# Optimization experiments

Hardware: AMD Instinct MI355X
Metric: run time of the kernel (lower is better)

Reference implementation:

```python
import jax, jax.numpy as jnp
import numpy as np

N_HEAD, D_MODEL, D_K, D_V = 16, 1024, 64, 64
B, L = 8, 1024
NEG = -1000000000.0
EPS = 1e-6


def setup_inputs() -> dict:
    key = jax.random.key(0)
    ks = jax.random.split(key, 8)
    s = 0.02
    return {
        "q": jax.random.normal(ks[0], (B, L, D_MODEL), jnp.float32),
        "k": jax.random.normal(ks[1], (B, L, D_MODEL), jnp.float32),
        "v": jax.random.normal(ks[2], (B, L, D_MODEL), jnp.float32),
        "mask": jnp.ones((B, L, L), jnp.int32),
        "w_q": jax.random.normal(ks[3], (D_MODEL, N_HEAD * D_K), jnp.float32) * s,
        "w_k": jax.random.normal(ks[4], (D_MODEL, N_HEAD * D_K), jnp.float32) * s,
        "w_v": jax.random.normal(ks[5], (D_MODEL, N_HEAD * D_V), jnp.float32) * s,
        "w_o": jax.random.normal(ks[6], (N_HEAD * D_V, D_MODEL), jnp.float32) * s,
        "gamma": jnp.ones((D_MODEL,), jnp.float32),
        "beta": jnp.zeros((D_MODEL,), jnp.float32),
    }


def reference(q, k, v, mask, w_q, w_k, w_v, w_o, gamma, beta):
    residual = q
    scale = D_K ** 0.5
    # project and split heads: [B, H, L, d]
    qh = (q @ w_q).reshape(B, L, N_HEAD, D_K).transpose(0, 2, 1, 3)
    kh = (k @ w_k).reshape(B, L, N_HEAD, D_K).transpose(0, 2, 1, 3)
    vh = (v @ w_v).reshape(B, L, N_HEAD, D_V).transpose(0, 2, 1, 3)
    scores = jnp.einsum('bhqd,bhkd->bhqk', qh / scale, kh)
    scores = jnp.where(mask[:, None, :, :] == 0, NEG, scores)
    attn = jax.nn.softmax(scores, axis=-1)  # dropout = identity (eval)
    ctx = jnp.einsum('bhqk,bhkd->bhqd', attn, vh)
    ctx = ctx.transpose(0, 2, 1, 3).reshape(B, L, N_HEAD * D_V)
    out = ctx @ w_o + residual
    mu = jnp.mean(out, axis=-1, keepdims=True)
    var = jnp.var(out, axis=-1, keepdims=True)
    out = (out - mu) / jnp.sqrt(var + EPS) * gamma + beta
    return out, attn
```

## Files before the change

### kernel.cpp

```cpp
#include <hip/hip_runtime.h>

typedef __bf16 bf16_t;
typedef __bf16 bf16x8 __attribute__((ext_vector_type(8)));
typedef float f32x4 __attribute__((ext_vector_type(4)));

#define MFMA16(a, b, c) __builtin_amdgcn_mfma_f32_16x16x32_bf16((a), (b), (c), 0, 0, 0)

__device__ __forceinline__ bf16_t f2b(float f) { return (bf16_t)f; }

__global__ __launch_bounds__(256) void prep_kernel(
    const float* __restrict__ w0, const float* __restrict__ w1,
    const float* __restrict__ w2, const float* __restrict__ w3,
    bf16_t* __restrict__ WT)
{
    int z = blockIdx.z;
    const float* W = (z == 0) ? w0 : (z == 1) ? w1 : (z == 2) ? w2 : w3;
    bf16_t* dst = WT + ((size_t)z << 20);
    __shared__ float lds[64 * 65];
    int n0 = blockIdx.x * 64, c0 = blockIdx.y * 64;
    int t = threadIdx.x;
    int rl = t >> 2, q4 = t & 3;
    const float* src = W + (size_t)(c0 + rl) * 1024 + n0 + q4 * 16;
    float4 a0 = *(const float4*)(src);
    float4 a1 = *(const float4*)(src + 4);
    float4 a2 = *(const float4*)(src + 8);
    float4 a3 = *(const float4*)(src + 12);
    float* lr = lds + rl * 65 + q4 * 16;
    lr[0] = a0.x; lr[1] = a0.y; lr[2] = a0.z; lr[3] = a0.w;
    lr[4] = a1.x; lr[5] = a1.y; lr[6] = a1.z; lr[7] = a1.w;
    lr[8] = a2.x; lr[9] = a2.y; lr[10] = a2.z; lr[11] = a2.w;
    lr[12] = a3.x; lr[13] = a3.y; lr[14] = a3.z; lr[15] = a3.w;
    __syncthreads();
    bf16x8 o0, o1;
#pragma unroll
    for (int j = 0; j < 8; ++j) o0[j] = f2b(lds[(q4 * 16 + j) * 65 + rl]);
#pragma unroll
    for (int j = 0; j < 8; ++j) o1[j] = f2b(lds[(q4 * 16 + 8 + j) * 65 + rl]);
    bf16_t* dp = dst + (size_t)(n0 + rl) * 1024 + c0 + q4 * 16;
    *(bf16x8*)(dp) = o0;
    *(bf16x8*)(dp + 8) = o1;
}

__global__ __launch_bounds__(256) void gemm_kernel(
    const float* __restrict__ Aq, const float* __restrict__ Ak,
    const float* __restrict__ Av, const bf16_t* __restrict__ Actx,
    const bf16_t* __restrict__ WT,
    bf16_t* __restrict__ oq, bf16_t* __restrict__ ok, bf16_t* __restrict__ ovT,
    float* __restrict__ otmp, int mode_base)
{
    int mode = mode_base + blockIdx.z;
    const float* Af = (mode == 0) ? Aq : (mode == 1) ? Ak : Av;
    const bf16_t* Wp = WT + ((size_t)mode << 20);
    __shared__ __align__(16) unsigned char sm[16384];
    int m0 = blockIdx.y * 128, n0 = blockIdx.x * 128;
    int t = threadIdx.x;
    int srow = t >> 1, shalf = t & 1;
    int wv = t >> 6, lane = t & 63, lrow = lane & 15, g = lane >> 4;
    int wm = (wv >> 1) * 64, wn = (wv & 1) * 64;
    f32x4 acc[4][4] = {};
    for (int kt = 0; kt < 32; ++kt) {
        int k0 = kt * 32;
        __syncthreads();
        {
            unsigned sab = srow * 64;
            int ch0 = (shalf * 2) ^ (srow & 3), ch1 = (shalf * 2 + 1) ^ (srow & 3);
            if (mode < 3) {
                const float* s = Af + (size_t)(m0 + srow) * 1024 + k0 + shalf * 16;
                float4 f0 = *(const float4*)(s);
                float4 f1 = *(const float4*)(s + 4);
                float4 f2 = *(const float4*)(s + 8);
                float4 f3 = *(const float4*)(s + 12);
                bf16x8 p0 = {f2b(f0.x), f2b(f0.y), f2b(f0.z), f2b(f0.w),
                             f2b(f1.x), f2b(f1.y), f2b(f1.z), f2b(f1.w)};
                bf16x8 p1 = {f2b(f2.x), f2b(f2.y), f2b(f2.z), f2b(f2.w),
                             f2b(f3.x), f2b(f3.y), f2b(f3.z), f2b(f3.w)};
                *(bf16x8*)(sm + sab + ch0 * 16) = p0;
                *(bf16x8*)(sm + sab + ch1 * 16) = p1;
            } else {
                const bf16_t* s = Actx + (size_t)(m0 + srow) * 1024 + k0 + shalf * 16;
                *(bf16x8*)(sm + sab + ch0 * 16) = *(const bf16x8*)(s);
                *(bf16x8*)(sm + sab + ch1 * 16) = *(const bf16x8*)(s + 8);
            }
            const bf16_t* sb = Wp + (size_t)(n0 + srow) * 1024 + k0 + shalf * 16;
            *(bf16x8*)(sm + 8192 + sab + ch0 * 16) = *(const bf16x8*)(sb);
            *(bf16x8*)(sm + 8192 + sab + ch1 * 16) = *(const bf16x8*)(sb + 8);
        }
        __syncthreads();
        bf16x8 av[4], bv[4];
#pragma unroll
        for (int i = 0; i < 4; ++i) {
            int ra = wm + i * 16 + lrow;
            av[i] = *(const bf16x8*)(sm + ra * 64 + ((g ^ (ra & 3)) * 16));
            int rb = wn + i * 16 + lrow;
            bv[i] = *(const bf16x8*)(sm + 8192 + rb * 64 + ((g ^ (rb & 3)) * 16));
        }
#pragma unroll
        for (int i = 0; i < 4; ++i)
#pragma unroll
            for (int j = 0; j < 4; ++j)
                acc[i][j] = MFMA16(av[i], bv[j], acc[i][j]);
    }
#pragma unroll
    for (int i = 0; i < 4; ++i)
#pragma unroll
        for (int j = 0; j < 4; ++j)
#pragma unroll
            for (int r = 0; r < 4; ++r) {
                int m = m0 + wm + i * 16 + 4 * g + r;
                int n = n0 + wn + j * 16 + lrow;
                float vv = acc[i][j][r];
                if (mode == 3) {
                    otmp[(size_t)m * 1024 + n] = vv;
                } else {
                    int b = m >> 10, l = m & 1023, h = n >> 6, d = n & 63;
                    int bh = (b << 4) | h;
                    if (mode == 0)
                        oq[((size_t)bh * 1024 + l) * 64 + d] = f2b(vv);
                    else if (mode == 1)
                        ok[((size_t)bh * 1024 + l) * 64 + d] = f2b(vv);
                    else
                        ovT[(size_t)bh * 65536 + (size_t)(l >> 5) * 2048 + d * 32 + (l & 31)] = f2b(vv);
                }
            }
}

__global__ __launch_bounds__(512) void attn_kernel(
    const bf16_t* __restrict__ wq, const bf16_t* __restrict__ wk,
    const bf16_t* __restrict__ wvT, const int* __restrict__ mask,
    float* __restrict__ attn, bf16_t* __restrict__ ctxo)
{
    __shared__ __align__(16) unsigned char sm[139264];
    int qt = blockIdx.x, bh = blockIdx.y;
    int b = bh >> 4, h = bh & 15;
    int t = threadIdx.x, wv = t >> 6, lane = t & 63, lrow = lane & 15, g = lane >> 4;
    const bf16_t* Kb = wk + (size_t)bh * 65536;
#pragma unroll
    for (int it = 0; it < 16; ++it) {
        int cid = it * 512 + t;
        int krow = cid >> 3, ch = cid & 7;
        *(bf16x8*)(sm + krow * 128 + ((ch ^ (krow & 7)) * 16)) =
            *(const bf16x8*)(Kb + krow * 64 + ch * 8);
    }
    __syncthreads();
    int q0 = qt * 128 + wv * 16;
    const bf16_t* Qb = wq + ((size_t)bh * 1024 + q0 + lrow) * 64;
    bf16x8 aq0 = *(const bf16x8*)(Qb + 8 * g);
    bf16x8 aq1 = *(const bf16x8*)(Qb + 32 + 8 * g);
    const int* mrow = mask + ((size_t)b * 1024 + q0) * 1024;
    f32x4 zf = {0.f, 0.f, 0.f, 0.f};
    float denom[4] = {0.f, 0.f, 0.f, 0.f};
    for (int kt = 0; kt < 64; ++kt) {
        int kc = kt * 16 + lrow;
        unsigned kb = kc * 128;
        bf16x8 bk0 = *(const bf16x8*)(sm + kb + ((g ^ (kc & 7)) * 16));
        bf16x8 bk1 = *(const bf16x8*)(sm + kb + (((4 + g) ^ (kc & 7)) * 16));
        f32x4 s = MFMA16(aq0, bk0, zf);
        s = MFMA16(aq1, bk1, s);
#pragma unroll
        for (int r = 0; r < 4; ++r) {
            float e = mrow[(size_t)(4 * g + r) * 1024 + kc] ? __expf(0.125f * s[r]) : 0.f;
            denom[r] += e;
        }
    }
#pragma unroll
    for (int r = 0; r < 4; ++r) {
        float e = denom[r];
        e += __shfl_xor(e, 1);
        e += __shfl_xor(e, 2);
        e += __shfl_xor(e, 4);
        e += __shfl_xor(e, 8);
        denom[r] = e;
    }
    float inv[4];
#pragma unroll
    for (int r = 0; r < 4; ++r) inv[r] = denom[r] > 0.f ? 1.f / denom[r] : 0.f;
    float* Ao = attn + ((size_t)bh * 1024 + q0) * 1024;
    const bf16_t* Vb = wvT + (size_t)bh * 65536;
    unsigned pb = 131072 + wv * 1024;
    f32x4 cacc[4] = {};
    for (int k2 = 0; k2 < 32; ++k2) {
#pragma unroll
        for (int f = 0; f < 2; ++f) {
            int kc = k2 * 32 + f * 16 + lrow;
            unsigned kb = kc * 128;
            bf16x8 bk0 = *(const bf16x8*)(sm + kb + ((g ^ (kc & 7)) * 16));
            bf16x8 bk1 = *(const bf16x8*)(sm + kb + (((4 + g) ^ (kc & 7)) * 16));
            f32x4 s = MFMA16(aq0, bk0, zf);
            s = MFMA16(aq1, bk1, s);
#pragma unroll
            for (int r = 0; r < 4; ++r) {
                int qr = 4 * g + r;
                float p = mrow[(size_t)qr * 1024 + kc] ? __expf(0.125f * s[r]) * inv[r] : 0.f;
                Ao[(size_t)qr * 1024 + kc] = p;
                int colw = f * 16 + lrow;
                unsigned byt = pb + qr * 64 + (((colw >> 3) ^ (qr & 3)) * 16) + (colw & 7) * 2;
                *(bf16_t*)(sm + byt) = f2b(p);
            }
        }
        __syncthreads();
        bf16x8 ap = *(const bf16x8*)(sm + pb + lrow * 64 + ((g ^ (lrow & 3)) * 16));
#pragma unroll
        for (int dt = 0; dt < 4; ++dt) {
            bf16x8 bv = *(const bf16x8*)(Vb + k2 * 2048 + (dt * 16 + lrow) * 32 + 8 * g);
            cacc[dt] = MFMA16(ap, bv, cacc[dt]);
        }
    }
    bf16_t* Co = ctxo + ((size_t)b * 1024 + q0) * 1024 + h * 64;
#pragma unroll
    for (int dt = 0; dt < 4; ++dt)
#pragma unroll
        for (int r = 0; r < 4; ++r)
            Co[(size_t)(4 * g + r) * 1024 + dt * 16 + lrow] = f2b(cacc[dt][r]);
}

__global__ __launch_bounds__(256) void ln_kernel(
    const float* __restrict__ tmp, const float* __restrict__ resid,
    const float* __restrict__ gamma, const float* __restrict__ beta,
    float* __restrict__ out)
{
    int row = blockIdx.x, t = threadIdx.x;
    const float4 x = *(const float4*)(tmp + (size_t)row * 1024 + t * 4);
    const float4 rs = *(const float4*)(resid + (size_t)row * 1024 + t * 4);
    float v0 = x.x + rs.x, v1 = x.y + rs.y, v2 = x.z + rs.z, v3 = x.w + rs.w;
    float s = v0 + v1 + v2 + v3;
    float q = v0 * v0 + v1 * v1 + v2 * v2 + v3 * v3;
#pragma unroll
    for (int m = 1; m < 64; m <<= 1) {
        s += __shfl_xor(s, m);
        q += __shfl_xor(q, m);
    }
    __shared__ float ps[4], pq[4];
    int wv = t >> 6;
    if ((t & 63) == 0) { ps[wv] = s; pq[wv] = q; }
    __syncthreads();
    s = ps[0] + ps[1] + ps[2] + ps[3];
    q = pq[0] + pq[1] + pq[2] + pq[3];
    float mean = s * (1.f / 1024.f);
    float var = q * (1.f / 1024.f) - mean * mean;
    float rstd = rsqrtf(var + 1e-6f);
    const float4 gm = *(const float4*)(gamma + t * 4);
    const float4 bt = *(const float4*)(beta + t * 4);
    float4 o;
    o.x = (v0 - mean) * rstd * gm.x + bt.x;
    o.y = (v1 - mean) * rstd * gm.y + bt.y;
    o.z = (v2 - mean) * rstd * gm.z + bt.z;
    o.w = (v3 - mean) * rstd * gm.w + bt.w;
    *(float4*)(out + (size_t)row * 1024 + t * 4) = o;
}

extern "C" void kernel_launch(void* const* d_in, const int* in_sizes, int n_in,
                              void* d_out, int out_size, void* d_ws, size_t ws_size,
                              hipStream_t stream) {
    const float* q = (const float*)d_in[0];
    const float* k = (const float*)d_in[1];
    const float* v = (const float*)d_in[2];
    const int* mask = (const int*)d_in[3];
    const float* w_q = (const float*)d_in[4];
    const float* w_k = (const float*)d_in[5];
    const float* w_v = (const float*)d_in[6];
    const float* w_o = (const float*)d_in[7];
    const float* gamma = (const float*)d_in[8];
    const float* beta = (const float*)d_in[9];
    float* out = (float*)d_out;
    float* attn = out + (size_t)8 * 1024 * 1024;

    unsigned char* ws = (unsigned char*)d_ws;
    bf16_t* ws_q = (bf16_t*)(ws);
    bf16_t* ws_k = (bf16_t*)(ws + 16777216);
    bf16_t* ws_vT = (bf16_t*)(ws + 33554432);
    bf16_t* ws_ctx = (bf16_t*)(ws + 50331648);
    bf16_t* WT = (bf16_t*)(ws + 67108864);
    float* tmp = (float*)(ws);

    prep_kernel<<<dim3(16, 16, 4), 256, 0, stream>>>(w_q, w_k, w_v, w_o, WT);
    gemm_kernel<<<dim3(8, 64, 3), 256, 0, stream>>>(q, k, v, nullptr, WT,
                                                    ws_q, ws_k, ws_vT, nullptr, 0);
    attn_kernel<<<dim3(8, 128), 512, 0, stream>>>(ws_q, ws_k, ws_vT, mask, attn, ws_ctx);
    gemm_kernel<<<dim3(8, 64, 1), 256, 0, stream>>>(nullptr, nullptr, nullptr, ws_ctx, WT,
                                                    nullptr, nullptr, nullptr, tmp, 3);
    ln_kernel<<<8192, 256, 0, stream>>>(tmp, q, gamma, beta, out);
}
```

Before: 1.133 ms.

## Use direct global-to-LDS loads in GEMM and bit-pack mask in attention

The GEMM now issues global_load_lds DMA copies of raw fp32 or bf16 tiles into a larger 64-wide K tile, converting fp32 to bf16 at LDS-read time instead of staging through registers. The attention kernel drops the 128 KB K staging in LDS, reads K directly from global memory, and packs the int32 mask for its 128-row tile into bitmasks in LDS. It also removes the per-iteration block barrier before the P·V step. This cuts LDS footprint to raise occupancy and reduces the mask read traffic. The trade-off is redundant K reads from cache and possible races, since the P tile is written and read within a wave without any barrier.

```diff
diff --git a/kernel.cpp b/kernel.cpp
--- a/kernel.cpp
+++ b/kernel.cpp
@@ -7,6 +7,12 @@
 #define MFMA16(a, b, c) __builtin_amdgcn_mfma_f32_16x16x32_bf16((a), (b), (c), 0, 0, 0)
 
 __device__ __forceinline__ bf16_t f2b(float f) { return (bf16_t)f; }
+
+__device__ __forceinline__ void gl_lds16(const void* g, void* l) {
+    __builtin_amdgcn_global_load_lds(
+        (const __attribute__((address_space(1))) void*)g,
+        (__attribute__((address_space(3))) void*)l, 16, 0, 0);
+}
 
 __global__ __launch_bounds__(256) void prep_kernel(
     const float* __restrict__ w0, const float* __restrict__ w1,
@@ -51,54 +57,66 @@
     int mode = mode_base + blockIdx.z;
     const float* Af = (mode == 0) ? Aq : (mode == 1) ? Ak : Av;
     const bf16_t* Wp = WT + ((size_t)mode << 20);
-    __shared__ __align__(16) unsigned char sm[16384];
+    __shared__ __align__(16) unsigned char sm[49152];
     int m0 = blockIdx.y * 128, n0 = blockIdx.x * 128;
-    int t = threadIdx.x;
-    int srow = t >> 1, shalf = t & 1;
-    int wv = t >> 6, lane = t & 63, lrow = lane & 15, g = lane >> 4;
+    int t = threadIdx.x, wv = t >> 6, lane = t & 63, lrow = lane & 15, g = lane >> 4;
     int wm = (wv >> 1) * 64, wn = (wv & 1) * 64;
     f32x4 acc[4][4] = {};
-    for (int kt = 0; kt < 32; ++kt) {
-        int k0 = kt * 32;
+    for (int kt = 0; kt < 16; ++kt) {
+        int k0 = kt * 64;
         __syncthreads();
-        {
-            unsigned sab = srow * 64;
-            int ch0 = (shalf * 2) ^ (srow & 3), ch1 = (shalf * 2 + 1) ^ (srow & 3);
-            if (mode < 3) {
-                const float* s = Af + (size_t)(m0 + srow) * 1024 + k0 + shalf * 16;
-                float4 f0 = *(const float4*)(s);
-                float4 f1 = *(const float4*)(s + 4);
-                float4 f2 = *(const float4*)(s + 8);
-                float4 f3 = *(const float4*)(s + 12);
-                bf16x8 p0 = {f2b(f0.x), f2b(f0.y), f2b(f0.z), f2b(f0.w),
-                             f2b(f1.x), f2b(f1.y), f2b(f1.z), f2b(f1.w)};
-                bf16x8 p1 = {f2b(f2.x), f2b(f2.y), f2b(f2.z), f2b(f2.w),
-                             f2b(f3.x), f2b(f3.y), f2b(f3.z), f2b(f3.w)};
-                *(bf16x8*)(sm + sab + ch0 * 16) = p0;
-                *(bf16x8*)(sm + sab + ch1 * 16) = p1;
-            } else {
-                const bf16_t* s = Actx + (size_t)(m0 + srow) * 1024 + k0 + shalf * 16;
-                *(bf16x8*)(sm + sab + ch0 * 16) = *(const bf16x8*)(s);
-                *(bf16x8*)(sm + sab + ch1 * 16) = *(const bf16x8*)(s + 8);
-            }
-            const bf16_t* sb = Wp + (size_t)(n0 + srow) * 1024 + k0 + shalf * 16;
-            *(bf16x8*)(sm + 8192 + sab + ch0 * 16) = *(const bf16x8*)(sb);
-            *(bf16x8*)(sm + 8192 + sab + ch1 * 16) = *(const bf16x8*)(sb + 8);
+        if (mode < 3) {
+#pragma unroll
+            for (int j = 0; j < 8; ++j) {
+                int ci = j * 256 + t;
+                int row = ci >> 4, c = ci & 15;
+                gl_lds16(Af + (size_t)(m0 + row) * 1024 + k0 + ((c ^ (row & 15)) << 2),
+                         sm + j * 4096 + wv * 1024);
+            }
+        } else {
+#pragma unroll
+            for (int j = 0; j < 4; ++j) {
+                int ci = j * 256 + t;
+                int row = ci >> 3, c = ci & 7;
+                gl_lds16(Actx + (size_t)(m0 + row) * 1024 + k0 + ((c ^ (row & 7)) << 3),
+                         sm + j * 4096 + wv * 1024);
+            }
+        }
+#pragma unroll
+        for (int j = 0; j < 4; ++j) {
+            int ci = j * 256 + t;
+            int row = ci >> 3, c = ci & 7;
+            gl_lds16(Wp + (size_t)(n0 + row) * 1024 + k0 + ((c ^ (row & 7)) << 3),
+                     sm + 32768 + j * 4096 + wv * 1024);
         }
         __syncthreads();
-        bf16x8 av[4], bv[4];
-#pragma unroll
-        for (int i = 0; i < 4; ++i) {
-            int ra = wm + i * 16 + lrow;
-            av[i] = *(const bf16x8*)(sm + ra * 64 + ((g ^ (ra & 3)) * 16));
-            int rb = wn + i * 16 + lrow;
-            bv[i] = *(const bf16x8*)(sm + 8192 + rb * 64 + ((g ^ (rb & 3)) * 16));
-        }
-#pragma unroll
-        for (int i = 0; i < 4; ++i)
-#pragma unroll
-            for (int j = 0; j < 4; ++j)
-                acc[i][j] = MFMA16(av[i], bv[j], acc[i][j]);
+#pragma unroll
+        for (int win = 0; win < 2; ++win) {
+            bf16x8 av[4], bv[4];
+#pragma unroll
+            for (int i = 0; i < 4; ++i) {
+                int ra = wm + i * 16 + lrow;
+                if (mode < 3) {
+                    int c0 = win * 8 + g * 2;
+                    f32x4 lo = *(const f32x4*)(sm + ra * 256 + (((c0) ^ (ra & 15)) * 16));
+                    f32x4 hi = *(const f32x4*)(sm + ra * 256 + (((c0 + 1) ^ (ra & 15)) * 16));
+                    bf16x8 fa = {f2b(lo[0]), f2b(lo[1]), f2b(lo[2]), f2b(lo[3]),
+                                 f2b(hi[0]), f2b(hi[1]), f2b(hi[2]), f2b(hi[3])};
+                    av[i] = fa;
+                } else {
+                    int c = win * 4 + g;
+                    av[i] = *(const bf16x8*)(sm + ra * 128 + ((c ^ (ra & 7)) * 16));
+                }
+                int rb = wn + i * 16 + lrow;
+                int cb = win * 4 + g;
+                bv[i] = *(const bf16x8*)(sm + 32768 + rb * 128 + ((cb ^ (rb & 7)) * 16));
+            }
+#pragma unroll
+            for (int i = 0; i < 4; ++i)
+#pragma unroll
+                for (int j2 = 0; j2 < 4; ++j2)
+                    acc[i][j2] = MFMA16(av[i], bv[j2], acc[i][j2]);
+        }
     }
 #pragma unroll
     for (int i = 0; i < 4; ++i)
@@ -129,37 +147,54 @@
     const bf16_t* __restrict__ wvT, const int* __restrict__ mask,
     float* __restrict__ attn, bf16_t* __restrict__ ctxo)
 {
-    __shared__ __align__(16) unsigned char sm[139264];
+    __shared__ __align__(16) unsigned char sm[24576];
+    unsigned* mbits = (unsigned*)sm;
     int qt = blockIdx.x, bh = blockIdx.y;
     int b = bh >> 4, h = bh & 15;
     int t = threadIdx.x, wv = t >> 6, lane = t & 63, lrow = lane & 15, g = lane >> 4;
-    const bf16_t* Kb = wk + (size_t)bh * 65536;
-#pragma unroll
-    for (int it = 0; it < 16; ++it) {
-        int cid = it * 512 + t;
-        int krow = cid >> 3, ch = cid & 7;
-        *(bf16x8*)(sm + krow * 128 + ((ch ^ (krow & 7)) * 16)) =
-            *(const bf16x8*)(Kb + krow * 64 + ch * 8);
+    {
+        const int4* mp = (const int4*)(mask + ((size_t)b << 20) + (size_t)qt * 128 * 1024);
+#pragma unroll
+        for (int it = 0; it < 8; ++it) {
+            int wi = it * 512 + t;
+            const int4* p = mp + wi * 8;
+            unsigned bits = 0;
+#pragma unroll
+            for (int c2 = 0; c2 < 8; ++c2) {
+                int4 mv = p[c2];
+                bits |= (mv.x != 0 ? 1u : 0u) << (c2 * 4);
+                bits |= (mv.y != 0 ? 1u : 0u) << (c2 * 4 + 1);
+                bits |= (mv.z != 0 ? 1u : 0u) << (c2 * 4 + 2);
+                bits |= (mv.w != 0 ? 1u : 0u) << (c2 * 4 + 3);
+            }
+            mbits[wi] = bits;
+        }
     }
     __syncthreads();
     int q0 = qt * 128 + wv * 16;
     const bf16_t* Qb = wq + ((size_t)bh * 1024 + q0 + lrow) * 64;
     bf16x8 aq0 = *(const bf16x8*)(Qb + 8 * g);
     bf16x8 aq1 = *(const bf16x8*)(Qb + 32 + 8 * g);
-    const int* mrow = mask + ((size_t)b * 1024 + q0) * 1024;
+    const bf16_t* Kb = wk + (size_t)bh * 65536;
+    const unsigned* mrow = mbits + (wv * 16 + 4 * g) * 32;
     f32x4 zf = {0.f, 0.f, 0.f, 0.f};
     float denom[4] = {0.f, 0.f, 0.f, 0.f};
-    for (int kt = 0; kt < 64; ++kt) {
-        int kc = kt * 16 + lrow;
-        unsigned kb = kc * 128;
-        bf16x8 bk0 = *(const bf16x8*)(sm + kb + ((g ^ (kc & 7)) * 16));
-        bf16x8 bk1 = *(const bf16x8*)(sm + kb + (((4 + g) ^ (kc & 7)) * 16));
-        f32x4 s = MFMA16(aq0, bk0, zf);
-        s = MFMA16(aq1, bk1, s);
+    for (int kp = 0; kp < 32; ++kp) {
+        int kcA = kp * 32 + lrow;
+        bf16x8 k0a = *(const bf16x8*)(Kb + (size_t)kcA * 64 + 8 * g);
+        bf16x8 k1a = *(const bf16x8*)(Kb + (size_t)kcA * 64 + 32 + 8 * g);
+        bf16x8 k0b = *(const bf16x8*)(Kb + (size_t)(kcA + 16) * 64 + 8 * g);
+        bf16x8 k1b = *(const bf16x8*)(Kb + (size_t)(kcA + 16) * 64 + 32 + 8 * g);
+        f32x4 sA = MFMA16(aq0, k0a, zf);
+        sA = MFMA16(aq1, k1a, sA);
+        f32x4 sB = MFMA16(aq0, k0b, zf);
+        sB = MFMA16(aq1, k1b, sB);
 #pragma unroll
         for (int r = 0; r < 4; ++r) {
-            float e = mrow[(size_t)(4 * g + r) * 1024 + kc] ? __expf(0.125f * s[r]) : 0.f;
-            denom[r] += e;
+            unsigned w = mrow[r * 32 + kp];
+            float mA = ((w >> lrow) & 1u) ? 1.f : 0.f;
+            float mB = ((w >> (16 + lrow)) & 1u) ? 1.f : 0.f;
+            denom[r] += mA * __expf(0.125f * sA[r]) + mB * __expf(0.125f * sB[r]);
         }
     }
 #pragma unroll
@@ -176,33 +211,38 @@
     for (int r = 0; r < 4; ++r) inv[r] = denom[r] > 0.f ? 1.f / denom[r] : 0.f;
     float* Ao = attn + ((size_t)bh * 1024 + q0) * 1024;
     const bf16_t* Vb = wvT + (size_t)bh * 65536;
-    unsigned pb = 131072 + wv * 1024;
+    unsigned pb = 16384 + wv * 1024;
     f32x4 cacc[4] = {};
     for (int k2 = 0; k2 < 32; ++k2) {
-#pragma unroll
-        for (int f = 0; f < 2; ++f) {
-            int kc = k2 * 32 + f * 16 + lrow;
-            unsigned kb = kc * 128;
-            bf16x8 bk0 = *(const bf16x8*)(sm + kb + ((g ^ (kc & 7)) * 16));
-            bf16x8 bk1 = *(const bf16x8*)(sm + kb + (((4 + g) ^ (kc & 7)) * 16));
-            f32x4 s = MFMA16(aq0, bk0, zf);
-            s = MFMA16(aq1, bk1, s);
-#pragma unroll
-            for (int r = 0; r < 4; ++r) {
-                int qr = 4 * g + r;
-                float p = mrow[(size_t)qr * 1024 + kc] ? __expf(0.125f * s[r]) * inv[r] : 0.f;
-                Ao[(size_t)qr * 1024 + kc] = p;
-                int colw = f * 16 + lrow;
-                unsigned byt = pb + qr * 64 + (((colw >> 3) ^ (qr & 3)) * 16) + (colw & 7) * 2;
-                *(bf16_t*)(sm + byt) = f2b(p);
-            }
-        }
-        __syncthreads();
+        int kcA = k2 * 32 + lrow;
+        bf16x8 k0a = *(const bf16x8*)(Kb + (size_t)kcA * 64 + 8 * g);
+        bf16x8 k1a = *(const bf16x8*)(Kb + (size_t)kcA * 64 + 32 + 8 * g);
+        bf16x8 k0b = *(const bf16x8*)(Kb + (size_t)(kcA + 16) * 64 + 8 * g);
+        bf16x8 k1b = *(const bf16x8*)(Kb + (size_t)(kcA + 16) * 64 + 32 + 8 * g);
+        f32x4 sA = MFMA16(aq0, k0a, zf);
+        sA = MFMA16(aq1, k1a, sA);
+        f32x4 sB = MFMA16(aq0, k0b, zf);
+        sB = MFMA16(aq1, k1b, sB);
+#pragma unroll
+        for (int r = 0; r < 4; ++r) {
+            int qr = 4 * g + r;
+            unsigned w = mrow[r * 32 + k2];
+            float mA = ((w >> lrow) & 1u) ? inv[r] : 0.f;
+            float mB = ((w >> (16 + lrow)) & 1u) ? inv[r] : 0.f;
+            float pA = __expf(0.125f * sA[r]) * mA;
+            float pB = __expf(0.125f * sB[r]) * mB;
+            Ao[(size_t)qr * 1024 + kcA] = pA;
+            Ao[(size_t)qr * 1024 + kcA + 16] = pB;
+            unsigned chA = (unsigned)((lrow >> 3) ^ (qr & 3));
+            unsigned chB = (unsigned)((2 + (lrow >> 3)) ^ (qr & 3));
+            *(bf16_t*)(sm + pb + qr * 64 + chA * 16 + (lrow & 7) * 2) = f2b(pA);
+            *(bf16_t*)(sm + pb + qr * 64 + chB * 16 + (lrow & 7) * 2) = f2b(pB);
+        }
         bf16x8 ap = *(const bf16x8*)(sm + pb + lrow * 64 + ((g ^ (lrow & 3)) * 16));
 #pragma unroll
         for (int dt = 0; dt < 4; ++dt) {
-            bf16x8 bv = *(const bf16x8*)(Vb + k2 * 2048 + (dt * 16 + lrow) * 32 + 8 * g);
-            cacc[dt] = MFMA16(ap, bv, cacc[dt]);
+            bf16x8 bvv = *(const bf16x8*)(Vb + (size_t)k2 * 2048 + (dt * 16 + lrow) * 32 + 8 * g);
+            cacc[dt] = MFMA16(ap, bvv, cacc[dt]);
         }
     }
     bf16_t* Co = ctxo + ((size_t)b * 1024 + q0) * 1024 + h * 64;
```

Result: slower. 1.157 ms (+2.1%).
